# Kernel tuning notes

Hardware: AMD Instinct MI355X
Metric: run time of the kernel (lower is better)

## Reference

```python
import jax, jax.numpy as jnp
import numpy as np

N_NODES = 50000
N_EDGES = 800000
IN_DIM = 128
OUT_DIM = 64


def setup_inputs() -> dict:
    key = jax.random.key(0)
    k1, k2, k3, k4, k5 = jax.random.split(key, 5)
    x = jax.random.normal(k1, (N_NODES, IN_DIM), dtype=jnp.float32)
    # Glorot-uniform-ish init for the GCN weight (weight_variable_glorot)
    limit = np.sqrt(6.0 / (IN_DIM + OUT_DIM)).astype(np.float32)
    weight = jax.random.uniform(k2, (IN_DIM, OUT_DIM), dtype=jnp.float32,
                                minval=-limit, maxval=limit)
    adj_row = jax.random.randint(k3, (N_EDGES,), 0, N_NODES, dtype=jnp.int32)
    adj_col = jax.random.randint(k4, (N_EDGES,), 0, N_NODES, dtype=jnp.int32)
    adj_val = jax.random.uniform(k5, (N_EDGES,), dtype=jnp.float32)
    return {"x": x, "weight": weight, "adj_row": adj_row,
            "adj_col": adj_col, "adj_val": adj_val}


def reference(x, weight, adj_row, adj_col, adj_val):
    # x: [N, F_in], weight: [F_in, F_out]; dropout=0.0 (default) is identity.
    xw = jnp.matmul(x, weight)                      # [N, F_out] dense GEMM
    # spmm(adj, xw) with adj in COO: gather neighbor feats, scale, scatter-add
    msg = adj_val[:, None] * xw[adj_col]            # [E, F_out]
    agg = jax.ops.segment_sum(msg, adj_row, num_segments=x.shape[0])  # [N, F_out]
    return jax.nn.relu(agg)
```

## Files before the change

kernel.cpp:

```cpp
#include <hip/hip_runtime.h>

#define IN_DIM 128
#define OUT_DIM 64
#define PADK 136
#define RB 64
#define RBSH 6
#define CAPB 1280
#define AB2 256

typedef float f32x4 __attribute__((ext_vector_type(4)));
typedef short bf16x8 __attribute__((ext_vector_type(8)));

__device__ __forceinline__ unsigned short f2bf(float f) {
    unsigned u = __float_as_uint(f);
    return (unsigned short)((u + 0x7FFFu + ((u >> 16) & 1u)) >> 16);
}
__device__ __forceinline__ float bf2f(unsigned short h) {
    return __uint_as_float((unsigned)h << 16);
}

__device__ __forceinline__ void gemm_body(const float* __restrict__ x,
                                          const float* __restrict__ w,
                                          unsigned short* __restrict__ xwb,
                                          int N, int blk,
                                          unsigned short* lds) {
    unsigned short* Ahi = lds;
    unsigned short* Alo = lds + 64 * PADK;
    unsigned short* Bhi = lds + 2 * 64 * PADK;
    unsigned short* Blo = lds + 3 * 64 * PADK;

    const int t = threadIdx.x;
    const int r0 = blk * 64;

    {
        const int c = t >> 2;
        const int kb = (t & 3) * 32;
        for (int k4 = 0; k4 < 32; k4 += 4) {
            ushort4 h, l;
            float v0 = w[(kb + k4 + 0) * OUT_DIM + c];
            float v1 = w[(kb + k4 + 1) * OUT_DIM + c];
            float v2 = w[(kb + k4 + 2) * OUT_DIM + c];
            float v3 = w[(kb + k4 + 3) * OUT_DIM + c];
            h.x = f2bf(v0); l.x = f2bf(v0 - bf2f(h.x));
            h.y = f2bf(v1); l.y = f2bf(v1 - bf2f(h.y));
            h.z = f2bf(v2); l.z = f2bf(v2 - bf2f(h.z));
            h.w = f2bf(v3); l.w = f2bf(v3 - bf2f(h.w));
            *(ushort4*)&Bhi[c * PADK + kb + k4] = h;
            *(ushort4*)&Blo[c * PADK + kb + k4] = l;
        }
    }
    {
        const float4* x4 = (const float4*)x;
        for (int i = 0; i < 8; ++i) {
            const int f = i * 256 + t;
            const int rr = f >> 5;
            const int kk = (f & 31) * 4;
            int row = r0 + rr; if (row >= N) row = N - 1;
            float4 v = x4[(size_t)row * (IN_DIM / 4) + (kk >> 2)];
            ushort4 h, l;
            h.x = f2bf(v.x); l.x = f2bf(v.x - bf2f(h.x));
            h.y = f2bf(v.y); l.y = f2bf(v.y - bf2f(h.y));
            h.z = f2bf(v.z); l.z = f2bf(v.z - bf2f(h.z));
            h.w = f2bf(v.w); l.w = f2bf(v.w - bf2f(h.w));
            *(ushort4*)&Ahi[rr * PADK + kk] = h;
            *(ushort4*)&Alo[rr * PADK + kk] = l;
        }
    }
    __syncthreads();

    const int lane = t & 63;
    const int wv = t >> 6;
    const int m = lane & 15;
    const int quad = lane >> 4;

    bf16x8 ahi[4], alo[4];
#pragma unroll
    for (int ks = 0; ks < 4; ++ks) {
        const int off = (wv * 16 + m) * PADK + ks * 32 + quad * 8;
        ahi[ks] = *(const bf16x8*)&Ahi[off];
        alo[ks] = *(const bf16x8*)&Alo[off];
    }
#pragma unroll
    for (int ct = 0; ct < 4; ++ct) {
        f32x4 acc = {0.f, 0.f, 0.f, 0.f};
#pragma unroll
        for (int ks = 0; ks < 4; ++ks) {
            const int off = (ct * 16 + m) * PADK + ks * 32 + quad * 8;
            bf16x8 bh = *(const bf16x8*)&Bhi[off];
            bf16x8 bl = *(const bf16x8*)&Blo[off];
            acc = __builtin_amdgcn_mfma_f32_16x16x32_bf16(alo[ks], bh, acc, 0, 0, 0);
            acc = __builtin_amdgcn_mfma_f32_16x16x32_bf16(ahi[ks], bl, acc, 0, 0, 0);
            acc = __builtin_amdgcn_mfma_f32_16x16x32_bf16(ahi[ks], bh, acc, 0, 0, 0);
        }
#pragma unroll
        for (int i = 0; i < 4; ++i) {
            const int row = r0 + wv * 16 + quad * 4 + i;
            if (row < N) xwb[(size_t)row * OUT_DIM + ct * 16 + m] = f2bf(acc[i]);
        }
    }
}

__device__ __forceinline__ void afill_body(
        const int* __restrict__ arow, const int* __restrict__ acol,
        const float* __restrict__ aval, int* __restrict__ pcur,
        int* __restrict__ ocount, uint4* __restrict__ olist,
        uint2* __restrict__ payload, int E, int NB, int chunk, int blk,
        int* ldsi) {
    int* cnt  = ldsi;
    int* base = ldsi + 1024;
    const int t = threadIdx.x;
    const int lo = blk * chunk;
    const int hi = min(E, lo + chunk);
    if (lo >= hi) return;
    const int len = hi - lo;
    const int n4  = len >> 2;
    const int4*   ar4 = (const int4*)(arow + lo);
    const int4*   ac4 = (const int4*)(acol + lo);
    const float4* av4 = (const float4*)(aval + lo);

    for (int i = t; i < NB; i += 256) cnt[i] = 0;
    __syncthreads();

    for (int j = t; j < n4; j += 256) {
        const int4 r = ar4[j];
        atomicAdd(&cnt[r.x >> RBSH], 1);
        atomicAdd(&cnt[r.y >> RBSH], 1);
        atomicAdd(&cnt[r.z >> RBSH], 1);
        atomicAdd(&cnt[r.w >> RBSH], 1);
    }
    for (int e = lo + (n4 << 2) + t; e < hi; e += 256)
        atomicAdd(&cnt[arow[e] >> RBSH], 1);
    __syncthreads();

    for (int i = t; i < NB; i += 256) {
        const int c = cnt[i];
        base[i] = c ? atomicAdd(&pcur[i], c) : 0;
        cnt[i] = 0;
    }
    __syncthreads();

#define AF_EMIT(RR, CC, VV) do {                                              \
        const int b_ = (RR) >> RBSH;                                          \
        const int slot_ = base[b_] + atomicAdd(&cnt[b_], 1);                  \
        const unsigned w0_ = (unsigned)(CC) |                                 \
                             ((unsigned)((RR) & (RB - 1)) << 16);             \
        const unsigned w1_ = __float_as_uint(VV);                             \
        if (slot_ < CAPB) {                                                   \
            payload[(size_t)b_ * CAPB + slot_] = make_uint2(w0_, w1_);        \
        } else {                                                              \
            const int oi_ = atomicAdd(ocount, 1);                             \
            olist[oi_] = make_uint4((unsigned)(RR), (unsigned)(CC), w1_, 0u); \
        }                                                                     \
    } while (0)

    for (int j = t; j < n4; j += 256) {
        const int4   r = ar4[j];
        const int4   c = ac4[j];
        const float4 v = av4[j];
        AF_EMIT(r.x, c.x, v.x);
        AF_EMIT(r.y, c.y, v.y);
        AF_EMIT(r.z, c.z, v.z);
        AF_EMIT(r.w, c.w, v.w);
    }
    for (int e = lo + (n4 << 2) + t; e < hi; e += 256)
        AF_EMIT(arow[e], acol[e], aval[e]);
#undef AF_EMIT
}

__global__ __launch_bounds__(256) void gemm_afill(
        const float* __restrict__ x, const float* __restrict__ w,
        unsigned short* __restrict__ xwb, int N,
        const int* __restrict__ arow, const int* __restrict__ acol,
        const float* __restrict__ aval, int* __restrict__ pcur,
        int* __restrict__ ocount, uint4* __restrict__ olist,
        uint2* __restrict__ payload, int E, int NB, int chunk) {
    __shared__ unsigned short LB[4 * 64 * PADK];
    if ((int)blockIdx.x < AB2) {
        afill_body(arow, acol, aval, pcur, ocount, olist, payload, E, NB,
                   chunk, blockIdx.x, (int*)LB);
    } else {
        gemm_body(x, w, xwb, N, blockIdx.x - AB2, LB);
    }
}

__global__ __launch_bounds__(256) void gemm_only(const float* __restrict__ x,
                                                 const float* __restrict__ w,
                                                 unsigned short* __restrict__ xwb,
                                                 int N) {
    __shared__ unsigned short LB[4 * 64 * PADK];
    gemm_body(x, w, xwb, N, blockIdx.x, LB);
}

__global__ __launch_bounds__(512) void bagg3(
        const int* __restrict__ pcur, const uint2* __restrict__ payload,
        const unsigned short* __restrict__ xwb, float* __restrict__ out, int N,
        const int* __restrict__ ocount, const uint4* __restrict__ olist) {
    __shared__ uint2 stage[CAPB];
    __shared__ int bins[RB + 1];
    __shared__ int pl[RB];
    const int t = threadIdx.x;
    const int lane = t & 63;
    const int wv = t >> 6;
    const int b = blockIdx.x;
    const int r0 = b << RBSH;

    const int cnt = min(pcur[b], CAPB);
    if (t <= RB) bins[t] = 0;
    if (t < RB) pl[t] = 0;
    __syncthreads();

    const uint2* pay = payload + (size_t)b * CAPB;
    for (int i = t; i < cnt; i += 512)
        atomicAdd(&bins[(pay[i].x >> 16) & (RB - 1)], 1);
    __syncthreads();
    if (t < RB) {
        const int v = bins[t];
        int s = v;
#pragma unroll
        for (int d = 1; d < RB; d <<= 1) {
            const int u = __shfl_up(s, d, 64);
            if (t >= d) s += u;
        }
        bins[t + 1] = s;
        if (t == 0) bins[0] = 0;
    }
    __syncthreads();
    for (int i = t; i < cnt; i += 512) {
        const uint2 e = pay[i];
        const int rl = (e.x >> 16) & (RB - 1);
        stage[bins[rl] + atomicAdd(&pl[rl], 1)] = e;
    }
    __syncthreads();

    float acc[8];
#pragma unroll
    for (int lr = 0; lr < 8; ++lr) {
        const int row = wv * 8 + lr;
        int j = bins[row];
        const int end = bins[row + 1];
        float a0 = 0.f, a1 = 0.f;
        for (; j + 8 <= end; j += 8) {
            uint2 e0 = stage[j],   e1 = stage[j+1], e2 = stage[j+2], e3 = stage[j+3];
            uint2 e4 = stage[j+4], e5 = stage[j+5], e6 = stage[j+6], e7 = stage[j+7];
            float g0 = bf2f(xwb[(size_t)(e0.x & 0xFFFF) * OUT_DIM + lane]);
            float g1 = bf2f(xwb[(size_t)(e1.x & 0xFFFF) * OUT_DIM + lane]);
            float g2 = bf2f(xwb[(size_t)(e2.x & 0xFFFF) * OUT_DIM + lane]);
            float g3 = bf2f(xwb[(size_t)(e3.x & 0xFFFF) * OUT_DIM + lane]);
            float g4 = bf2f(xwb[(size_t)(e4.x & 0xFFFF) * OUT_DIM + lane]);
            float g5 = bf2f(xwb[(size_t)(e5.x & 0xFFFF) * OUT_DIM + lane]);
            float g6 = bf2f(xwb[(size_t)(e6.x & 0xFFFF) * OUT_DIM + lane]);
            float g7 = bf2f(xwb[(size_t)(e7.x & 0xFFFF) * OUT_DIM + lane]);
            a0 = fmaf(__uint_as_float(e0.y), g0, a0);
            a1 = fmaf(__uint_as_float(e1.y), g1, a1);
            a0 = fmaf(__uint_as_float(e2.y), g2, a0);
            a1 = fmaf(__uint_as_float(e3.y), g3, a1);
            a0 = fmaf(__uint_as_float(e4.y), g4, a0);
            a1 = fmaf(__uint_as_float(e5.y), g5, a1);
            a0 = fmaf(__uint_as_float(e6.y), g6, a0);
            a1 = fmaf(__uint_as_float(e7.y), g7, a1);
        }
        for (; j + 4 <= end; j += 4) {
            uint2 e0 = stage[j], e1 = stage[j+1], e2 = stage[j+2], e3 = stage[j+3];
            float g0 = bf2f(xwb[(size_t)(e0.x & 0xFFFF) * OUT_DIM + lane]);
            float g1 = bf2f(xwb[(size_t)(e1.x & 0xFFFF) * OUT_DIM + lane]);
            float g2 = bf2f(xwb[(size_t)(e2.x & 0xFFFF) * OUT_DIM + lane]);
            float g3 = bf2f(xwb[(size_t)(e3.x & 0xFFFF) * OUT_DIM + lane]);
            a0 = fmaf(__uint_as_float(e0.y), g0, a0);
            a1 = fmaf(__uint_as_float(e1.y), g1, a1);
            a0 = fmaf(__uint_as_float(e2.y), g2, a0);
            a1 = fmaf(__uint_as_float(e3.y), g3, a1);
        }
        for (; j < end; ++j) {
            uint2 e0 = stage[j];
            a0 = fmaf(__uint_as_float(e0.y),
                      bf2f(xwb[(size_t)(e0.x & 0xFFFF) * OUT_DIM + lane]), a0);
        }
        acc[lr] = a0 + a1;
    }

    const int oc = *ocount;
    for (int i = 0; i < oc; ++i) {
        const uint4 e = olist[i];
        const int lr = (int)e.x - r0 - wv * 8;
        if (lr >= 0 && lr < 8)
            acc[lr] += __uint_as_float(e.z) *
                       bf2f(xwb[(size_t)e.y * OUT_DIM + lane]);
    }

#pragma unroll
    for (int lr = 0; lr < 8; ++lr) {
        const int row = r0 + wv * 8 + lr;
        if (row < N) {
            const float v = acc[lr];
            out[(size_t)row * OUT_DIM + lane] = v > 0.f ? v : 0.f;
        }
    }
}

__global__ __launch_bounds__(256) void scatter_edges(
        const int* __restrict__ arow, const int* __restrict__ acol,
        const float* __restrict__ aval, const unsigned short* __restrict__ xwb,
        float* __restrict__ out, int E) {
    const int lane = threadIdx.x & 63;
    int gw = (blockIdx.x * 256 + (int)threadIdx.x) >> 6;
    const int nw = (gridDim.x * 256) >> 6;
    for (int e = gw; e < E; e += nw) {
        const float m = aval[e] * bf2f(xwb[(size_t)acol[e] * OUT_DIM + lane]);
        atomicAdd(&out[(size_t)arow[e] * OUT_DIM + lane], m);
    }
}

__global__ __launch_bounds__(256) void relu_inplace(float* __restrict__ o, int n4) {
    float4* p = (float4*)o;
    int i = blockIdx.x * 256 + threadIdx.x;
    const int stride = gridDim.x * 256;
    for (; i < n4; i += stride) {
        float4 v = p[i];
        v.x = v.x > 0.f ? v.x : 0.f;
        v.y = v.y > 0.f ? v.y : 0.f;
        v.z = v.z > 0.f ? v.z : 0.f;
        v.w = v.w > 0.f ? v.w : 0.f;
        p[i] = v;
    }
}

static inline size_t align256(size_t x) { return (x + 255) & ~(size_t)255; }

extern "C" void kernel_launch(void* const* d_in, const int* in_sizes, int n_in,
                              void* d_out, int out_size, void* d_ws, size_t ws_size,
                              hipStream_t stream) {
    const float* x    = (const float*)d_in[0];
    const float* w    = (const float*)d_in[1];
    const int*   arow = (const int*)d_in[2];
    const int*   acol = (const int*)d_in[3];
    const float* aval = (const float*)d_in[4];
    float*       out  = (float*)d_out;

    const int N  = in_sizes[0] / IN_DIM;
    const int E  = in_sizes[2];
    const int NB = (N + RB - 1) >> RBSH;
    const int GB = (N + 63) / 64;

    char* ws = (char*)d_ws;
    const size_t szXW  = align256((size_t)N * OUT_DIM * sizeof(unsigned short));
    const size_t szCnt = align256((size_t)(NB + 1) * sizeof(int));
    const size_t szOl  = align256((size_t)E * sizeof(uint4));
    const size_t szPay = (size_t)NB * CAPB * sizeof(uint2);
    const size_t need0 = szXW + szCnt + szOl + szPay;

    unsigned short* xwb = (unsigned short*)ws;
    int*   pcur    = (int*)(ws + szXW);
    int*   ocount  = pcur + NB;
    uint4* olist   = (uint4*)(ws + szXW + szCnt);
    uint2* payload = (uint2*)(ws + szXW + szCnt + szOl);

    if (ws_size >= need0 && N <= 65536 && NB <= 1024) {
        (void)hipMemsetAsync(pcur, 0, (size_t)(NB + 1) * sizeof(int), stream);
        const int chunk = (((E + AB2 - 1) / AB2) + 3) & ~3;
        gemm_afill<<<AB2 + GB, 256, 0, stream>>>(x, w, xwb, N, arow, acol, aval,
                                                 pcur, ocount, olist, payload,
                                                 E, NB, chunk);
        bagg3<<<NB, 512, 0, stream>>>(pcur, payload, xwb, out, N, ocount, olist);
    } else {
        gemm_only<<<GB, 256, 0, stream>>>(x, w, xwb, N);
        (void)hipMemsetAsync(d_out, 0, (size_t)out_size * sizeof(float), stream);
        scatter_edges<<<4096, 256, 0, stream>>>(arow, acol, aval, xwb, out, E);
        relu_inplace<<<2048, 256, 0, stream>>>(out, out_size / 4);
    }
}
```

Baseline: 123.5 us.

## Bucket edges per row with global atomics and load GEMM A directly to registers

Edge bucketing now happens per destination row rather than per 64-row block. Each edge takes a slot from a global atomic counter for its row and is written to a fixed 48-entry slot in that row's payload. This removes the two-pass LDS histogram in the fill kernel and the in-block counting sort in the aggregation kernel. The GEMM now loads x rows straight into registers and splits them into bf16 hi/lo there, which removes the A-tile LDS staging and halves shared memory. In exchange it adds many contended global atomics and a larger sparse payload buffer, and rows with more than 48 edges spill to the slow overflow list.

Measured after the change: 155.2 us. +25.6%, slower.

```diff
diff --git a/kernel.cpp b/kernel.cpp
--- a/kernel.cpp
+++ b/kernel.cpp
@@ -5,7 +5,7 @@
 #define PADK 136
 #define RB 64
 #define RBSH 6
-#define CAPB 1280
+#define CAPR 48
 #define AB2 256
 
 typedef float f32x4 __attribute__((ext_vector_type(4)));
@@ -24,10 +24,8 @@
                                           unsigned short* __restrict__ xwb,
                                           int N, int blk,
                                           unsigned short* lds) {
-    unsigned short* Ahi = lds;
-    unsigned short* Alo = lds + 64 * PADK;
-    unsigned short* Bhi = lds + 2 * 64 * PADK;
-    unsigned short* Blo = lds + 3 * 64 * PADK;
+    unsigned short* Bhi = lds;
+    unsigned short* Blo = lds + 64 * PADK;
 
     const int t = threadIdx.x;
     const int r0 = blk * 64;
@@ -49,37 +47,31 @@
             *(ushort4*)&Blo[c * PADK + kb + k4] = l;
         }
     }
-    {
-        const float4* x4 = (const float4*)x;
-        for (int i = 0; i < 8; ++i) {
-            const int f = i * 256 + t;
-            const int rr = f >> 5;
-            const int kk = (f & 31) * 4;
-            int row = r0 + rr; if (row >= N) row = N - 1;
-            float4 v = x4[(size_t)row * (IN_DIM / 4) + (kk >> 2)];
-            ushort4 h, l;
-            h.x = f2bf(v.x); l.x = f2bf(v.x - bf2f(h.x));
-            h.y = f2bf(v.y); l.y = f2bf(v.y - bf2f(h.y));
-            h.z = f2bf(v.z); l.z = f2bf(v.z - bf2f(h.z));
-            h.w = f2bf(v.w); l.w = f2bf(v.w - bf2f(h.w));
-            *(ushort4*)&Ahi[rr * PADK + kk] = h;
-            *(ushort4*)&Alo[rr * PADK + kk] = l;
-        }
-    }
-    __syncthreads();
 
     const int lane = t & 63;
     const int wv = t >> 6;
     const int m = lane & 15;
     const int quad = lane >> 4;
 
+    int row = r0 + wv * 16 + m; if (row >= N) row = N - 1;
+    const float4* xr = (const float4*)(x + (size_t)row * IN_DIM);
     bf16x8 ahi[4], alo[4];
 #pragma unroll
     for (int ks = 0; ks < 4; ++ks) {
-        const int off = (wv * 16 + m) * PADK + ks * 32 + quad * 8;
-        ahi[ks] = *(const bf16x8*)&Ahi[off];
-        alo[ks] = *(const bf16x8*)&Alo[off];
-    }
+        const float4 v0 = xr[ks * 8 + quad * 2];
+        const float4 v1 = xr[ks * 8 + quad * 2 + 1];
+        float f[8] = {v0.x, v0.y, v0.z, v0.w, v1.x, v1.y, v1.z, v1.w};
+        bf16x8 h8, l8;
+#pragma unroll
+        for (int i = 0; i < 8; ++i) {
+            const unsigned short h = f2bf(f[i]);
+            h8[i] = (short)h;
+            l8[i] = (short)f2bf(f[i] - bf2f(h));
+        }
+        ahi[ks] = h8; alo[ks] = l8;
+    }
+    __syncthreads();
+
 #pragma unroll
     for (int ct = 0; ct < 4; ++ct) {
         f32x4 acc = {0.f, 0.f, 0.f, 0.f};
@@ -94,20 +86,17 @@
         }
 #pragma unroll
         for (int i = 0; i < 4; ++i) {
-            const int row = r0 + wv * 16 + quad * 4 + i;
-            if (row < N) xwb[(size_t)row * OUT_DIM + ct * 16 + m] = f2bf(acc[i]);
+            const int r = r0 + wv * 16 + quad * 4 + i;
+            if (r < N) xwb[(size_t)r * OUT_DIM + ct * 16 + m] = f2bf(acc[i]);
         }
     }
 }
 
 __device__ __forceinline__ void afill_body(
         const int* __restrict__ arow, const int* __restrict__ acol,
-        const float* __restrict__ aval, int* __restrict__ pcur,
+        const float* __restrict__ aval, int* __restrict__ rowcnt,
         int* __restrict__ ocount, uint4* __restrict__ olist,
-        uint2* __restrict__ payload, int E, int NB, int chunk, int blk,
-        int* ldsi) {
-    int* cnt  = ldsi;
-    int* base = ldsi + 1024;
+        uint2* __restrict__ payload, int E, int chunk, int blk) {
     const int t = threadIdx.x;
     const int lo = blk * chunk;
     const int hi = min(E, lo + chunk);
@@ -118,38 +107,14 @@
     const int4*   ac4 = (const int4*)(acol + lo);
     const float4* av4 = (const float4*)(aval + lo);
 
-    for (int i = t; i < NB; i += 256) cnt[i] = 0;
-    __syncthreads();
-
-    for (int j = t; j < n4; j += 256) {
-        const int4 r = ar4[j];
-        atomicAdd(&cnt[r.x >> RBSH], 1);
-        atomicAdd(&cnt[r.y >> RBSH], 1);
-        atomicAdd(&cnt[r.z >> RBSH], 1);
-        atomicAdd(&cnt[r.w >> RBSH], 1);
-    }
-    for (int e = lo + (n4 << 2) + t; e < hi; e += 256)
-        atomicAdd(&cnt[arow[e] >> RBSH], 1);
-    __syncthreads();
-
-    for (int i = t; i < NB; i += 256) {
-        const int c = cnt[i];
-        base[i] = c ? atomicAdd(&pcur[i], c) : 0;
-        cnt[i] = 0;
-    }
-    __syncthreads();
-
-#define AF_EMIT(RR, CC, VV) do {                                              \
-        const int b_ = (RR) >> RBSH;                                          \
-        const int slot_ = base[b_] + atomicAdd(&cnt[b_], 1);                  \
-        const unsigned w0_ = (unsigned)(CC) |                                 \
-                             ((unsigned)((RR) & (RB - 1)) << 16);             \
-        const unsigned w1_ = __float_as_uint(VV);                             \
-        if (slot_ < CAPB) {                                                   \
-            payload[(size_t)b_ * CAPB + slot_] = make_uint2(w0_, w1_);        \
+#define AF_EMIT(RR, CC, VV, SS) do {                                          \
+        if ((SS) < CAPR) {                                                    \
+            payload[(size_t)(RR) * CAPR + (SS)] =                             \
+                make_uint2((unsigned)(CC), __float_as_uint(VV));              \
         } else {                                                              \
             const int oi_ = atomicAdd(ocount, 1);                             \
-            olist[oi_] = make_uint4((unsigned)(RR), (unsigned)(CC), w1_, 0u); \
+            olist[oi_] = make_uint4((unsigned)(RR), (unsigned)(CC),           \
+                                    __float_as_uint(VV), 0u);                 \
         }                                                                     \
     } while (0)
 
@@ -157,13 +122,20 @@
         const int4   r = ar4[j];
         const int4   c = ac4[j];
         const float4 v = av4[j];
-        AF_EMIT(r.x, c.x, v.x);
-        AF_EMIT(r.y, c.y, v.y);
-        AF_EMIT(r.z, c.z, v.z);
-        AF_EMIT(r.w, c.w, v.w);
-    }
-    for (int e = lo + (n4 << 2) + t; e < hi; e += 256)
-        AF_EMIT(arow[e], acol[e], aval[e]);
+        const int s0 = atomicAdd(&rowcnt[r.x], 1);
+        const int s1 = atomicAdd(&rowcnt[r.y], 1);
+        const int s2 = atomicAdd(&rowcnt[r.z], 1);
+        const int s3 = atomicAdd(&rowcnt[r.w], 1);
+        AF_EMIT(r.x, c.x, v.x, s0);
+        AF_EMIT(r.y, c.y, v.y, s1);
+        AF_EMIT(r.z, c.z, v.z, s2);
+        AF_EMIT(r.w, c.w, v.w, s3);
+    }
+    for (int e = lo + (n4 << 2) + t; e < hi; e += 256) {
+        const int r = arow[e];
+        const int s = atomicAdd(&rowcnt[r], 1);
+        AF_EMIT(r, acol[e], aval[e], s);
+    }
 #undef AF_EMIT
 }
 
@@ -171,13 +143,13 @@
         const float* __restrict__ x, const float* __restrict__ w,
         unsigned short* __restrict__ xwb, int N,
         const int* __restrict__ arow, const int* __restrict__ acol,
-        const float* __restrict__ aval, int* __restrict__ pcur,
+        const float* __restrict__ aval, int* __restrict__ rowcnt,
         int* __restrict__ ocount, uint4* __restrict__ olist,
-        uint2* __restrict__ payload, int E, int NB, int chunk) {
-    __shared__ unsigned short LB[4 * 64 * PADK];
+        uint2* __restrict__ payload, int E, int chunk) {
+    __shared__ unsigned short LB[2 * 64 * PADK];
     if ((int)blockIdx.x < AB2) {
-        afill_body(arow, acol, aval, pcur, ocount, olist, payload, E, NB,
-                   chunk, blockIdx.x, (int*)LB);
+        afill_body(arow, acol, aval, rowcnt, ocount, olist, payload, E,
+                   chunk, blockIdx.x);
     } else {
         gemm_body(x, w, xwb, N, blockIdx.x - AB2, LB);
     }
@@ -187,48 +159,33 @@
                                                  const float* __restrict__ w,
                                                  unsigned short* __restrict__ xwb,
                                                  int N) {
-    __shared__ unsigned short LB[4 * 64 * PADK];
+    __shared__ unsigned short LB[2 * 64 * PADK];
     gemm_body(x, w, xwb, N, blockIdx.x, LB);
 }
 
-__global__ __launch_bounds__(512) void bagg3(
-        const int* __restrict__ pcur, const uint2* __restrict__ payload,
+__global__ __launch_bounds__(512) void bagg4(
+        const int* __restrict__ rowcnt, const uint2* __restrict__ payload,
         const unsigned short* __restrict__ xwb, float* __restrict__ out, int N,
         const int* __restrict__ ocount, const uint4* __restrict__ olist) {
-    __shared__ uint2 stage[CAPB];
-    __shared__ int bins[RB + 1];
-    __shared__ int pl[RB];
+    __shared__ uint2 stage[RB * CAPR];
+    __shared__ int cnts[RB];
     const int t = threadIdx.x;
     const int lane = t & 63;
     const int wv = t >> 6;
     const int b = blockIdx.x;
     const int r0 = b << RBSH;
 
-    const int cnt = min(pcur[b], CAPB);
-    if (t <= RB) bins[t] = 0;
-    if (t < RB) pl[t] = 0;
+    if (t < RB) {
+        const int r = r0 + t;
+        cnts[t] = (r < N) ? min(rowcnt[r], CAPR) : 0;
+    }
     __syncthreads();
 
-    const uint2* pay = payload + (size_t)b * CAPB;
-    for (int i = t; i < cnt; i += 512)
-        atomicAdd(&bins[(pay[i].x >> 16) & (RB - 1)], 1);
-    __syncthreads();
-    if (t < RB) {
-        const int v = bins[t];
-        int s = v;
-#pragma unroll
-        for (int d = 1; d < RB; d <<= 1) {
-            const int u = __shfl_up(s, d, 64);
-            if (t >= d) s += u;
-        }
-        bins[t + 1] = s;
-        if (t == 0) bins[0] = 0;
-    }
-    __syncthreads();
-    for (int i = t; i < cnt; i += 512) {
-        const uint2 e = pay[i];
-        const int rl = (e.x >> 16) & (RB - 1);
-        stage[bins[rl] + atomicAdd(&pl[rl], 1)] = e;
+    for (int rl = wv; rl < RB; rl += 8) {
+        const int c = cnts[rl];
+        const uint2* src = payload + (size_t)(r0 + rl) * CAPR;
+        for (int j = lane; j < c; j += 64)
+            stage[rl * CAPR + j] = src[j];
     }
     __syncthreads();
 
@@ -236,20 +193,20 @@
 #pragma unroll
     for (int lr = 0; lr < 8; ++lr) {
         const int row = wv * 8 + lr;
-        int j = bins[row];
-        const int end = bins[row + 1];
+        int j = row * CAPR;
+        const int end = j + cnts[row];
         float a0 = 0.f, a1 = 0.f;
         for (; j + 8 <= end; j += 8) {
             uint2 e0 = stage[j],   e1 = stage[j+1], e2 = stage[j+2], e3 = stage[j+3];
             uint2 e4 = stage[j+4], e5 = stage[j+5], e6 = stage[j+6], e7 = stage[j+7];
-            float g0 = bf2f(xwb[(size_t)(e0.x & 0xFFFF) * OUT_DIM + lane]);
-            float g1 = bf2f(xwb[(size_t)(e1.x & 0xFFFF) * OUT_DIM + lane]);
-            float g2 = bf2f(xwb[(size_t)(e2.x & 0xFFFF) * OUT_DIM + lane]);
-            float g3 = bf2f(xwb[(size_t)(e3.x & 0xFFFF) * OUT_DIM + lane]);
-            float g4 = bf2f(xwb[(size_t)(e4.x & 0xFFFF) * OUT_DIM + lane]);
-            float g5 = bf2f(xwb[(size_t)(e5.x & 0xFFFF) * OUT_DIM + lane]);
-            float g6 = bf2f(xwb[(size_t)(e6.x & 0xFFFF) * OUT_DIM + lane]);
-            float g7 = bf2f(xwb[(size_t)(e7.x & 0xFFFF) * OUT_DIM + lane]);
+            float g0 = bf2f(xwb[(size_t)e0.x * OUT_DIM + lane]);
+            float g1 = bf2f(xwb[(size_t)e1.x * OUT_DIM + lane]);
+            float g2 = bf2f(xwb[(size_t)e2.x * OUT_DIM + lane]);
+            float g3 = bf2f(xwb[(size_t)e3.x * OUT_DIM + lane]);
+            float g4 = bf2f(xwb[(size_t)e4.x * OUT_DIM + lane]);
+            float g5 = bf2f(xwb[(size_t)e5.x * OUT_DIM + lane]);
+            float g6 = bf2f(xwb[(size_t)e6.x * OUT_DIM + lane]);
+            float g7 = bf2f(xwb[(size_t)e7.x * OUT_DIM + lane]);
             a0 = fmaf(__uint_as_float(e0.y), g0, a0);
             a1 = fmaf(__uint_as_float(e1.y), g1, a1);
             a0 = fmaf(__uint_as_float(e2.y), g2, a0);
@@ -261,10 +218,10 @@
         }
         for (; j + 4 <= end; j += 4) {
             uint2 e0 = stage[j], e1 = stage[j+1], e2 = stage[j+2], e3 = stage[j+3];
-            float g0 = bf2f(xwb[(size_t)(e0.x & 0xFFFF) * OUT_DIM + lane]);
-            float g1 = bf2f(xwb[(size_t)(e1.x & 0xFFFF) * OUT_DIM + lane]);
-            float g2 = bf2f(xwb[(size_t)(e2.x & 0xFFFF) * OUT_DIM + lane]);
-            float g3 = bf2f(xwb[(size_t)(e3.x & 0xFFFF) * OUT_DIM + lane]);
+            float g0 = bf2f(xwb[(size_t)e0.x * OUT_DIM + lane]);
+            float g1 = bf2f(xwb[(size_t)e1.x * OUT_DIM + lane]);
+            float g2 = bf2f(xwb[(size_t)e2.x * OUT_DIM + lane]);
+            float g3 = bf2f(xwb[(size_t)e3.x * OUT_DIM + lane]);
             a0 = fmaf(__uint_as_float(e0.y), g0, a0);
             a1 = fmaf(__uint_as_float(e1.y), g1, a1);
             a0 = fmaf(__uint_as_float(e2.y), g2, a0);
@@ -273,7 +230,7 @@
         for (; j < end; ++j) {
             uint2 e0 = stage[j];
             a0 = fmaf(__uint_as_float(e0.y),
-                      bf2f(xwb[(size_t)(e0.x & 0xFFFF) * OUT_DIM + lane]), a0);
+                      bf2f(xwb[(size_t)e0.x * OUT_DIM + lane]), a0);
         }
         acc[lr] = a0 + a1;
     }
@@ -343,24 +300,24 @@
 
     char* ws = (char*)d_ws;
     const size_t szXW  = align256((size_t)N * OUT_DIM * sizeof(unsigned short));
-    const size_t szCnt = align256((size_t)(NB + 1) * sizeof(int));
+    const size_t szCnt = align256((size_t)(N + 1) * sizeof(int));
     const size_t szOl  = align256((size_t)E * sizeof(uint4));
-    const size_t szPay = (size_t)NB * CAPB * sizeof(uint2);
+    const size_t szPay = (size_t)N * CAPR * sizeof(uint2);
     const size_t need0 = szXW + szCnt + szOl + szPay;
 
     unsigned short* xwb = (unsigned short*)ws;
-    int*   pcur    = (int*)(ws + szXW);
-    int*   ocount  = pcur + NB;
+    int*   rowcnt  = (int*)(ws + szXW);
+    int*   ocount  = rowcnt + N;
     uint4* olist   = (uint4*)(ws + szXW + szCnt);
     uint2* payload = (uint2*)(ws + szXW + szCnt + szOl);
 
-    if (ws_size >= need0 && N <= 65536 && NB <= 1024) {
-        (void)hipMemsetAsync(pcur, 0, (size_t)(NB + 1) * sizeof(int), stream);
+    if (ws_size >= need0 && N <= 65536) {
+        (void)hipMemsetAsync(rowcnt, 0, (size_t)(N + 1) * sizeof(int), stream);
         const int chunk = (((E + AB2 - 1) / AB2) + 3) & ~3;
         gemm_afill<<<AB2 + GB, 256, 0, stream>>>(x, w, xwb, N, arow, acol, aval,
-                                                 pcur, ocount, olist, payload,
-                                                 E, NB, chunk);
-        bagg3<<<NB, 512, 0, stream>>>(pcur, payload, xwb, out, N, ocount, olist);
+                                                 rowcnt, ocount, olist, payload,
+                                                 E, chunk);
+        bagg4<<<NB, 512, 0, stream>>>(rowcnt, payload, xwb, out, N, ocount, olist);
     } else {
         gemm_only<<<GB, 256, 0, stream>>>(x, w, xwb, N);
         (void)hipMemsetAsync(d_out, 0, (size_t)out_size * sizeof(float), stream);
```

## Load GEMM A fragments directly from global into registers, halve LDS, more afill blocks

Applied to the files above, without the earlier changes.

The GEMM no longer stages x tiles through shared memory. Each lane reads its two float4s per k-step straight from global memory and splits them into hi/lo bf16 fragments in registers, so only the weight tile stays in LDS. This halves the static LDS footprint, which can raise occupancy for the fused gemm_afill kernel. AB2 doubles to 512, so the edge-fill phase is spread over twice as many blocks. The trade-off is uncoalesced-ish strided global loads for A, plus more afill blocks each doing smaller chunks with per-block overhead.

After: 139.1 us. 12.6% more time.

```diff
diff --git a/kernel.cpp b/kernel.cpp
--- a/kernel.cpp
+++ b/kernel.cpp
@@ -6,7 +6,7 @@
 #define RB 64
 #define RBSH 6
 #define CAPB 1280
-#define AB2 256
+#define AB2 512
 
 typedef float f32x4 __attribute__((ext_vector_type(4)));
 typedef short bf16x8 __attribute__((ext_vector_type(8)));
@@ -24,10 +24,8 @@
                                           unsigned short* __restrict__ xwb,
                                           int N, int blk,
                                           unsigned short* lds) {
-    unsigned short* Ahi = lds;
-    unsigned short* Alo = lds + 64 * PADK;
-    unsigned short* Bhi = lds + 2 * 64 * PADK;
-    unsigned short* Blo = lds + 3 * 64 * PADK;
+    unsigned short* Bhi = lds;
+    unsigned short* Blo = lds + 64 * PADK;
 
     const int t = threadIdx.x;
     const int r0 = blk * 64;
@@ -49,37 +47,31 @@
             *(ushort4*)&Blo[c * PADK + kb + k4] = l;
         }
     }
-    {
-        const float4* x4 = (const float4*)x;
-        for (int i = 0; i < 8; ++i) {
-            const int f = i * 256 + t;
-            const int rr = f >> 5;
-            const int kk = (f & 31) * 4;
-            int row = r0 + rr; if (row >= N) row = N - 1;
-            float4 v = x4[(size_t)row * (IN_DIM / 4) + (kk >> 2)];
-            ushort4 h, l;
-            h.x = f2bf(v.x); l.x = f2bf(v.x - bf2f(h.x));
-            h.y = f2bf(v.y); l.y = f2bf(v.y - bf2f(h.y));
-            h.z = f2bf(v.z); l.z = f2bf(v.z - bf2f(h.z));
-            h.w = f2bf(v.w); l.w = f2bf(v.w - bf2f(h.w));
-            *(ushort4*)&Ahi[rr * PADK + kk] = h;
-            *(ushort4*)&Alo[rr * PADK + kk] = l;
-        }
-    }
-    __syncthreads();
 
     const int lane = t & 63;
     const int wv = t >> 6;
     const int m = lane & 15;
     const int quad = lane >> 4;
 
+    int row = r0 + wv * 16 + m; if (row >= N) row = N - 1;
+    const float4* xr = (const float4*)(x + (size_t)row * IN_DIM);
     bf16x8 ahi[4], alo[4];
 #pragma unroll
     for (int ks = 0; ks < 4; ++ks) {
-        const int off = (wv * 16 + m) * PADK + ks * 32 + quad * 8;
-        ahi[ks] = *(const bf16x8*)&Ahi[off];
-        alo[ks] = *(const bf16x8*)&Alo[off];
-    }
+        const float4 v0 = xr[ks * 8 + quad * 2];
+        const float4 v1 = xr[ks * 8 + quad * 2 + 1];
+        float f[8] = {v0.x, v0.y, v0.z, v0.w, v1.x, v1.y, v1.z, v1.w};
+        bf16x8 h8, l8;
+#pragma unroll
+        for (int i = 0; i < 8; ++i) {
+            const unsigned short h = f2bf(f[i]);
+            h8[i] = (short)h;
+            l8[i] = (short)f2bf(f[i] - bf2f(h));
+        }
+        ahi[ks] = h8; alo[ks] = l8;
+    }
+    __syncthreads();
+
 #pragma unroll
     for (int ct = 0; ct < 4; ++ct) {
         f32x4 acc = {0.f, 0.f, 0.f, 0.f};
@@ -94,8 +86,8 @@
         }
 #pragma unroll
         for (int i = 0; i < 4; ++i) {
-            const int row = r0 + wv * 16 + quad * 4 + i;
-            if (row < N) xwb[(size_t)row * OUT_DIM + ct * 16 + m] = f2bf(acc[i]);
+            const int r = r0 + wv * 16 + quad * 4 + i;
+            if (r < N) xwb[(size_t)r * OUT_DIM + ct * 16 + m] = f2bf(acc[i]);
         }
     }
 }
@@ -174,7 +166,7 @@
         const float* __restrict__ aval, int* __restrict__ pcur,
         int* __restrict__ ocount, uint4* __restrict__ olist,
         uint2* __restrict__ payload, int E, int NB, int chunk) {
-    __shared__ unsigned short LB[4 * 64 * PADK];
+    __shared__ unsigned short LB[2 * 64 * PADK];
     if ((int)blockIdx.x < AB2) {
         afill_body(arow, acol, aval, pcur, ocount, olist, payload, E, NB,
                    chunk, blockIdx.x, (int*)LB);
@@ -187,7 +179,7 @@
                                                  const float* __restrict__ w,
                                                  unsigned short* __restrict__ xwb,
                                                  int N) {
-    __shared__ unsigned short LB[4 * 64 * PADK];
+    __shared__ unsigned short LB[2 * 64 * PADK];
     gemm_body(x, w, xwb, N, blockIdx.x, LB);
 }
 
```
